# Kernel optimization log

Measured on AMD Instinct MI355X. Metric: run time of the kernel, lower is better.

Reference implementation:

```python
import jax, jax.numpy as jnp
import numpy as np

NUM_PTM_TYPES = 26
NUM_PER_TYPE = 128
TEMPERATURE = 0.07


def setup_inputs() -> dict:
    key = jax.random.key(0)
    k1, k2, k3 = jax.random.split(key, 3)
    N, D = 8192, 256
    x = jax.random.normal(k1, (N, D), dtype=jnp.float32)
    Q = jax.random.randint(k2, (N,), 0, NUM_PTM_TYPES)
    E = jax.random.normal(k3, (NUM_PTM_TYPES * NUM_PER_TYPE, D), dtype=jnp.float32)
    E = E / jnp.linalg.norm(E, axis=1, keepdims=True)  # matches _initialize_embeddings
    return {"x": x, "Q": Q, "E": E, "tau": 1}


def _quantize_grouped(x, Q, E, tau):
    # Vectorized form of the per-PTM-type loop: every type owns an equal-size
    # sub-codebook of NUM_PER_TYPE rows, so gather each token's sub-codebook.
    D = x.shape[-1]
    cb = E.reshape(NUM_PTM_TYPES, NUM_PER_TYPE, D)[Q]          # [N, K, D]
    dot = jnp.einsum('nd,nkd->nk', x, cb) / tau                # [N, K]
    sim = jax.nn.softmax(dot, axis=-1)
    z_q = jnp.einsum('nk,nkd->nd', sim, cb)                    # [N, D]
    idx = jnp.argmax(sim, axis=-1) + Q * NUM_PER_TYPE          # global code index
    return z_q, idx


def _uniform_loss(E):
    K = E.shape[0]
    En = E / jnp.linalg.norm(E, axis=1, keepdims=True)
    sim = En @ En.T                                            # [K, K]
    labels = jnp.arange(K) // NUM_PER_TYPE
    labels_eq = labels[None, :] == labels[:, None]
    eye = jnp.eye(K, dtype=bool)
    sim = jnp.where(eye, -jnp.inf, sim)
    sim_exp = jnp.exp(sim / TEMPERATURE)                       # diagonal -> 0
    sum_exp = jnp.sum(sim_exp, axis=1)
    pos_sum_exp = jnp.sum(sim_exp * labels_eq.astype(sim_exp.dtype), axis=1)
    return -jnp.mean(jnp.log(pos_sum_exp / sum_exp))


def reference(x, Q, E, tau):
    tau = jnp.float32(tau)
    quantized, encoding_indices = _quantize_grouped(x, Q, E, tau)
    loss = jnp.float32(0.0)
    uniform_loss = _uniform_loss(E)
    return quantized, loss, uniform_loss, encoding_indices
```

## Files before the change

### kernel.cpp

```cpp
#include <hip/hip_runtime.h>
#include <hip/hip_bf16.h>

#define NUM_TYPES 26
#define NPT 128
#define DIMS 256
#define K_TOTAL 3328
#define N_TOK 8192
#define INV_TEMP (1.0f/0.07f)
#define TM 16
#define MAX_TILES 32
#define NHIST 32

typedef unsigned short ushort_t;
typedef short bf16x8 __attribute__((ext_vector_type(8)));
typedef float f32x4 __attribute__((ext_vector_type(4)));

__device__ __forceinline__ float wave_reduce_sum(float v){
#pragma unroll
  for (int off = 32; off; off >>= 1) v += __shfl_xor(v, off);
  return v;
}

__device__ __forceinline__ unsigned short f2bf(float f){
  __hip_bfloat16 h = __float2bfloat16(f);
  return __builtin_bit_cast(unsigned short, h);
}

#define GLOAD_LDS16(g, s) \
  __builtin_amdgcn_global_load_lds((__attribute__((address_space(1))) void*)(g), \
                                   (__attribute__((address_space(3))) void*)(s), 16, 0, 0)

#define VMWAIT(N) do{ asm volatile("s_waitcnt vmcnt(" #N ")" ::: "memory"); \
                      __builtin_amdgcn_sched_barrier(0); }while(0)

__global__ __launch_bounds__(256) void prepk(const float* __restrict__ E,
                                             const int* __restrict__ Q,
                                             ushort_t* __restrict__ Enb,
                                             float* __restrict__ EA2,
                                             ushort_t* __restrict__ EC,
                                             int* __restrict__ bh){
  const int t = threadIdx.x;
  const int b = blockIdx.x;
  if (b < 832){
    const int w = t >> 6, l = t & 63;
    const int row = b * 4 + w;
    float4 v = reinterpret_cast<const float4*>(E + (size_t)row * DIMS)[l];
    float ss = v.x*v.x + v.y*v.y + v.z*v.z + v.w*v.w;
    ss = wave_reduce_sum(ss);
    const float inv = 1.0f / sqrtf(ss);
    ushort4 o;
    o.x = f2bf(v.x * inv); o.y = f2bf(v.y * inv);
    o.z = f2bf(v.z * inv); o.w = f2bf(v.w * inv);
    reinterpret_cast<ushort4*>(Enb + (size_t)row * DIMS)[l] = o;
    return;
  }
  if (b < 936){
    const int id = b - 832;
    const int tp = id >> 2, ck = id & 3;
    __shared__ float T[32][260];
    const int row = t >> 3, sub = t & 7;
    const float* src = E + (size_t)(tp*NPT + ck*32 + row) * DIMS;
#pragma unroll
    for (int i = 0; i < 8; ++i){
      const int c4 = sub + 8*i;
      *(f32x4*)(&T[row][c4*4]) = *(const f32x4*)(src + c4*4);
    }
    __syncthreads();
    ushort_t* dst = EC + (size_t)(tp*4 + ck) * 8192;
#pragma unroll
    for (int i = 0; i < 4; ++i){
      const int si = t + i*256;
      const int sec = si >> 8, d = (si >> 2) & 63, s = si & 3;
      const int cb8 = (s ^ ((d >> 1) & 3)) * 8;
      union { bf16x8 v8; ushort_t u[8]; } pk;
#pragma unroll
      for (int j = 0; j < 8; ++j)
        pk.u[j] = f2bf(T[cb8 + j][sec*64 + d]);
      *(bf16x8*)(dst + (size_t)si*8) = pk.v8;
    }
    return;
  }
  if (b < 1144){
    const int id = b - 936;
    const int tp = id >> 3, kt = id & 7;
    float* dst = EA2 + (size_t)tp*32768 + kt*1024;
    const float* src = E + (size_t)tp * NPT * DIMS;
#pragma unroll
    for (int i = 0; i < 16; ++i){
      const int e = i*256 + t;
      const int sec = e >> 10, code = (e >> 3) & 127, j = e & 7;
      dst[sec*8192 + code*8 + j] = src[(size_t)code*DIMS + sec*64 + kt*8 + j];
    }
    return;
  }
  {
    __shared__ int h[NUM_TYPES];
    if (t < NUM_TYPES) h[t] = 0;
    __syncthreads();
    const int c = b - 1144;
    atomicAdd(&h[Q[c*256 + t]], 1);
    __syncthreads();
    if (t < NUM_TYPES) bh[c*NUM_TYPES + t] = h[t];
  }
}

__global__ __launch_bounds__(256) void gramk(const ushort_t* __restrict__ Enb,
                                             const int* __restrict__ Q,
                                             const int* __restrict__ bh,
                                             int* __restrict__ counts,
                                             int* __restrict__ offsets,
                                             int* __restrict__ perm,
                                             float* __restrict__ part){
  const int bi = blockIdx.y, bj = blockIdx.x;
  const int t = threadIdx.x;
  if (bi > bj){
    const int lid = bi*(bi-1)/2 + bj;
    if (lid >= NHIST) return;
    __shared__ int sh_tot[NUM_TYPES], sh_off[NUM_TYPES], sh_cur[NUM_TYPES];
    if (t < NUM_TYPES){
      int s = 0;
      for (int h = 0; h < NHIST; ++h) s += bh[h*NUM_TYPES + t];
      sh_tot[t] = s;
    }
    __syncthreads();
    if (t == 0){
      int s = 0;
      for (int g = 0; g < NUM_TYPES; ++g){ sh_off[g] = s; s += sh_tot[g]; }
    }
    __syncthreads();
    if (t < NUM_TYPES){
      int run = sh_off[t];
      for (int h = 0; h < lid; ++h) run += bh[h*NUM_TYPES + t];
      sh_cur[t] = run;
      if (lid == 0){ counts[t] = sh_tot[t]; offsets[t] = sh_off[t]; }
    }
    __syncthreads();
    const int i = lid*256 + t;
    const int q = Q[i];
    const int pos = atomicAdd(&sh_cur[q], 1);
    perm[pos] = i;
    return;
  }
  __shared__ ushort_t As[128*64];
  __shared__ ushort_t Bs[128*64];
  __shared__ float rs[128][2];
  __shared__ float cs[128][2];
  const int w = t >> 6, l = t & 63;
  const int wr = w >> 1, wc = w & 1;
  const int lrow = l & 15;
  const int lk = (l >> 4) * 8;
  const int hi = l >> 4;

  f32x4 acc[4][4];
#pragma unroll
  for (int m = 0; m < 4; ++m)
#pragma unroll
    for (int n = 0; n < 4; ++n) acc[m][n] = (f32x4){0.f, 0.f, 0.f, 0.f};

  for (int kt = 0; kt < 4; ++kt){
    if (kt) __syncthreads();
#pragma unroll
    for (int p = 0; p < 4; ++p){
      const int cbase = p*256 + w*64;
      const int c = cbase + l;
      const int row = c >> 3;
      const int kcol = (c & 7) * 8;
      const ushort_t* gA = Enb + (size_t)(bi*128 + row) * DIMS + kt*64 + kcol;
      const ushort_t* gB = Enb + (size_t)(bj*128 + row) * DIMS + kt*64 + kcol;
      GLOAD_LDS16(gA, As + (size_t)cbase*8);
      GLOAD_LDS16(gB, Bs + (size_t)cbase*8);
    }
    __syncthreads();
#pragma unroll
    for (int kk = 0; kk < 2; ++kk){
      bf16x8 a[4], b[4];
#pragma unroll
      for (int m = 0; m < 4; ++m)
        a[m] = *reinterpret_cast<const bf16x8*>(&As[(wr*64 + m*16 + lrow)*64 + kk*32 + lk]);
#pragma unroll
      for (int n = 0; n < 4; ++n)
        b[n] = *reinterpret_cast<const bf16x8*>(&Bs[(wc*64 + n*16 + lrow)*64 + kk*32 + lk]);
#pragma unroll
      for (int m = 0; m < 4; ++m)
#pragma unroll
        for (int n = 0; n < 4; ++n)
          acc[m][n] = __builtin_amdgcn_mfma_f32_16x16x32_bf16(a[m], b[n], acc[m][n], 0, 0, 0);
    }
  }

#pragma unroll
  for (int m = 0; m < 4; ++m)
#pragma unroll
    for (int n = 0; n < 4; ++n)
#pragma unroll
      for (int j = 0; j < 4; ++j){
        const int grow = bi*128 + wr*64 + m*16 + hi*4 + j;
        const int gcol = bj*128 + wc*64 + n*16 + lrow;
        const float g = acc[m][n][j];
        acc[m][n][j] = (grow == gcol) ? 0.f : __expf(g * INV_TEMP);
      }

#pragma unroll
  for (int m = 0; m < 4; ++m)
#pragma unroll
    for (int j = 0; j < 4; ++j){
      float s = 0.f;
#pragma unroll
      for (int n = 0; n < 4; ++n) s += acc[m][n][j];
#pragma unroll
      for (int off = 1; off < 16; off <<= 1) s += __shfl_xor(s, off);
      if (lrow == 0) rs[wr*64 + m*16 + hi*4 + j][wc] = s;
    }
  if (bi != bj){
#pragma unroll
    for (int n = 0; n < 4; ++n){
      float c = 0.f;
#pragma unroll
      for (int m = 0; m < 4; ++m)
#pragma unroll
        for (int j = 0; j < 4; ++j) c += acc[m][n][j];
      c += __shfl_xor(c, 16); c += __shfl_xor(c, 32);
      if (hi == 0) cs[wc*64 + n*16 + lrow][wr] = c;
    }
  }
  __syncthreads();
  if (t < 128){
    part[(size_t)bj*K_TOTAL + bi*128 + t] = rs[t][0] + rs[t][1];
    if (bi != bj)
      part[(size_t)bi*K_TOTAL + bj*128 + t] = cs[t][0] + cs[t][1];
  }
}

__device__ __forceinline__ void stageC3(const ushort_t* EC, char* dst, int tp, int ck,
                                        int w, int l){
  const char* src = (const char*)(EC + (size_t)(tp*4 + ck) * 8192) + w*4096;
  char* d = dst + w*4096;
#pragma unroll
  for (int i = 0; i < 4; ++i)
    GLOAD_LDS16(src + i*1024 + l*16, d + i*1024);
}

__global__ __launch_bounds__(256, 4) void quantg(const float* __restrict__ x,
                                                 const float* __restrict__ EA2,
                                                 const ushort_t* __restrict__ EC,
                                                 const float* __restrict__ part,
                                                 const int* __restrict__ counts,
                                                 const int* __restrict__ offsets,
                                                 const int* __restrict__ perm,
                                                 const int* __restrict__ taup,
                                                 float* __restrict__ outZ,
                                                 float* __restrict__ outMisc,
                                                 float* __restrict__ outIdx){
  const int t = threadIdx.x;
  const int tp = blockIdx.x, rb = blockIdx.y;
  __shared__ __align__(16) char arena[37120];

  if (tp == NUM_TYPES){
    if (rb) return;
    float acc = 0.f;
    for (int i = t; i < K_TOTAL; i += 256){
      float s = 0.f;
#pragma unroll
      for (int bb = 0; bb < NUM_TYPES; ++bb) s += part[(size_t)bb*K_TOTAL + i];
      acc += logf(s) - logf(part[(size_t)(i >> 7)*K_TOTAL + i]);
    }
    acc = wave_reduce_sum(acc);
    float* red = (float*)arena;
    if ((t & 63) == 0) red[t >> 6] = acc;
    __syncthreads();
    if (t == 0){ outMisc[0] = 0.f; outMisc[1] = (red[0]+red[1]+red[2]+red[3]) / (float)K_TOTAL; }
    return;
  }

  const int cnt = counts[tp];
  if (rb * TM >= cnt) return;
  const int nt = min(TM, cnt - rb * TM);
  const int off = offsets[tp] + rb * TM;

  char* XA = arena;
  char* PB = arena;
  char* BC = arena;
  char* SB = arena + 32768;

  const int w = t >> 6, l = t & 63;
  const int h  = w >> 1;
  const int cg = w & 1;
  const int tx = l & 15, ty = l >> 4;

  const int ti = *taup;
  const float tau = (ti > 0 && ti < (1 << 23)) ? (float)ti : __int_as_float(ti);
  const float inv_tau = 1.0f / tau;

#pragma unroll
  for (int i = 0; i < 4; ++i){
    const int row = w*4 + i;
    const int tid = (row < nt) ? perm[off + row] : perm[off];
    const int sc = (l & 56) | ((l & 7) ^ (row & 7));
    GLOAD_LDS16(x + (size_t)tid*DIMS + sc*4, XA + row*1024);
  }
  __syncthreads();

  float acc[4][4];
#pragma unroll
  for (int rr = 0; rr < 4; ++rr)
#pragma unroll
    for (int cc = 0; cc < 4; ++cc) acc[rr][cc] = 0.f;

  const float* ea = EA2 + (size_t)tp*32768 + h*16384;
#pragma unroll
  for (int kk = 0; kk < 16; ++kk){
    f32x4 b0[4], b1[4];
#pragma unroll
    for (int cc = 0; cc < 4; ++cc){
      const float* p = ea + (kk >> 3)*8192 + (kk & 7)*1024 + (size_t)(cg*64 + tx + 16*cc)*8;
      b0[cc] = *(const f32x4*)(p);
      b1[cc] = *(const f32x4*)(p + 4);
    }
#pragma unroll
    for (int q = 0; q < 2; ++q){
      f32x4 a[4];
#pragma unroll
      for (int rr = 0; rr < 4; ++rr){
        const int row = rr*4 + ty;
        const int c = (h*32 + kk*2 + q) ^ (row & 7);
        a[rr] = *(const f32x4*)(XA + row*1024 + c*16);
      }
#pragma unroll
      for (int rr = 0; rr < 4; ++rr)
#pragma unroll
        for (int cc = 0; cc < 4; ++cc)
#pragma unroll
          for (int e = 0; e < 4; ++e)
            acc[rr][cc] = fmaf(a[rr][e], (q ? b1 : b0)[cc][e], acc[rr][cc]);
    }
  }
  __syncthreads();

#pragma unroll
  for (int rr = 0; rr < 4; ++rr){
    const int row = rr*4 + ty;
#pragma unroll
    for (int cc = 0; cc < 4; ++cc)
      *(float*)(PB + h*8448 + row*528 + (cg*64 + tx + 16*cc)*4) = acc[rr][cc];
  }
  __syncthreads();

  {
    const int r = t >> 4, s = t & 15;
    f32x4 v0 = (f32x4){0,0,0,0}, v1 = (f32x4){0,0,0,0};
#pragma unroll
    for (int ww = 0; ww < 2; ++ww){
      v0 += *(const f32x4*)(PB + ww*8448 + r*528 + s*32);
      v1 += *(const f32x4*)(PB + ww*8448 + r*528 + s*32 + 16);
    }
    float v[8];
#pragma unroll
    for (int e = 0; e < 4; ++e){ v[e] = v0[e]*inv_tau; v[4+e] = v1[e]*inv_tau; }
    float m = v[0]; int mi = s*8;
#pragma unroll
    for (int j = 1; j < 8; ++j) if (v[j] > m){ m = v[j]; mi = s*8 + j; }
#pragma unroll
    for (int o = 1; o < 16; o <<= 1){
      const float om = __shfl_xor(m, o);
      const int   oi = __shfl_xor(mi, o);
      if (om > m || (om == m && oi < mi)){ m = om; mi = oi; }
    }
    float e8[8]; float sum = 0.f;
#pragma unroll
    for (int j = 0; j < 8; ++j){ e8[j] = __expf(v[j] - m); sum += e8[j]; }
#pragma unroll
    for (int o = 1; o < 16; o <<= 1) sum += __shfl_xor(sum, o);
    const float inv = 1.0f / sum;
    union { bf16x8 v8; ushort_t u[8]; } pk;
#pragma unroll
    for (int j = 0; j < 8; ++j) pk.u[j] = f2bf(e8[j] * inv);
    *(bf16x8*)(SB + r*272 + s*16) = pk.v8;
    if (s == 0 && r < nt)
      outIdx[perm[off + r]] = (float)(mi + tp * NPT);
  }
  __syncthreads();

  stageC3(EC, BC, tp, 0, w, l);
  f32x4 zacc[4];
#pragma unroll
  for (int n = 0; n < 4; ++n) zacc[n] = (f32x4){0,0,0,0};
#pragma unroll
  for (int ck = 0; ck < 4; ++ck){
    if (ck < 3) stageC3(EC, BC + ((ck+1)&1)*16384, tp, ck+1, w, l);
    if (ck < 3)      { VMWAIT(4); }
    else             { VMWAIT(0); }
    const bf16x8 af = *(const bf16x8*)(SB + tx*272 + ck*64 + ty*16);
    const char* bbuf = BC + (ck&1)*16384 + w*4096;
#pragma unroll
    for (int n = 0; n < 4; ++n){
      const int d = n*16 + tx;
      const int slot = ty ^ ((d >> 1) & 3);
      const bf16x8 bf = *(const bf16x8*)(bbuf + d*64 + slot*16);
      zacc[n] = __builtin_amdgcn_mfma_f32_16x16x32_bf16(af, bf, zacc[n], 0, 0, 0);
    }
  }
#pragma unroll
  for (int n = 0; n < 4; ++n)
#pragma unroll
    for (int j = 0; j < 4; ++j){
      const int row = ty*4 + j;
      if (row < nt)
        outZ[(size_t)perm[off + row]*DIMS + w*64 + n*16 + tx] = zacc[n][j];
    }
}

extern "C" void kernel_launch(void* const* d_in, const int* in_sizes, int n_in,
                              void* d_out, int out_size, void* d_ws, size_t ws_size,
                              hipStream_t stream){
  const float* x  = (const float*)d_in[0];
  const int*   Q  = (const int*)d_in[1];
  const float* E  = (const float*)d_in[2];
  const int* taup = (const int*)d_in[3];

  float* outZ    = (float*)d_out;
  float* outMisc = outZ + (size_t)N_TOK * DIMS;
  float* outIdx  = outMisc + 2;

  char* wsp = (char*)d_ws;
  ushort_t* Enb = (ushort_t*)wsp;
  float* part   = (float*)(wsp + 1703936);
  float* EA2    = (float*)(wsp + 2050048);
  ushort_t* EC  = (ushort_t*)(wsp + 5457920);
  int* bh       = (int*)(wsp + 7161856);
  int* counts   = (int*)(wsp + 7165184);
  int* offsets  = (int*)(wsp + 7165312);
  int* perm     = (int*)(wsp + 7165440);

  prepk<<<1176, 256, 0, stream>>>(E, Q, Enb, EA2, EC, bh);
  gramk<<<dim3(26, 26), 256, 0, stream>>>(Enb, Q, bh, counts, offsets, perm, part);
  quantg<<<dim3(NUM_TYPES + 1, MAX_TILES), 256, 0, stream>>>(x, EA2, EC, part,
                                                             counts, offsets, perm,
                                                             taup, outZ, outMisc, outIdx);
}
```

Measured before the change: 45.87 us.

## Move codebook layout prep into gram kernel idle blocks and parallelize loss reduction

The EC and EA2 codebook re-layout blocks move out of the first kernel and into otherwise idle lower-triangle blocks of the gram kernel, with the grid grown by one row so there are enough spare blocks. This shortens the critical first kernel and overlaps the layout work with the gram matmul. The final uniform-loss reduction is split across 26 blocks, and a threadfence plus atomic counter picks a last block to combine the partial sums, replacing a single serial block. The exchange is an extra memset launch and atomics, and gram tiles now use a shared arena sized for the largest use.

```diff
diff --git a/kernel.cpp b/kernel.cpp
--- a/kernel.cpp
+++ b/kernel.cpp
@@ -36,8 +36,6 @@
 __global__ __launch_bounds__(256) void prepk(const float* __restrict__ E,
                                              const int* __restrict__ Q,
                                              ushort_t* __restrict__ Enb,
-                                             float* __restrict__ EA2,
-                                             ushort_t* __restrict__ EC,
                                              int* __restrict__ bh){
   const int t = threadIdx.x;
   const int b = blockIdx.x;
@@ -54,97 +52,105 @@
     reinterpret_cast<ushort4*>(Enb + (size_t)row * DIMS)[l] = o;
     return;
   }
-  if (b < 936){
-    const int id = b - 832;
-    const int tp = id >> 2, ck = id & 3;
-    __shared__ float T[32][260];
-    const int row = t >> 3, sub = t & 7;
-    const float* src = E + (size_t)(tp*NPT + ck*32 + row) * DIMS;
-#pragma unroll
-    for (int i = 0; i < 8; ++i){
-      const int c4 = sub + 8*i;
-      *(f32x4*)(&T[row][c4*4]) = *(const f32x4*)(src + c4*4);
-    }
-    __syncthreads();
-    ushort_t* dst = EC + (size_t)(tp*4 + ck) * 8192;
-#pragma unroll
-    for (int i = 0; i < 4; ++i){
-      const int si = t + i*256;
-      const int sec = si >> 8, d = (si >> 2) & 63, s = si & 3;
-      const int cb8 = (s ^ ((d >> 1) & 3)) * 8;
-      union { bf16x8 v8; ushort_t u[8]; } pk;
-#pragma unroll
-      for (int j = 0; j < 8; ++j)
-        pk.u[j] = f2bf(T[cb8 + j][sec*64 + d]);
-      *(bf16x8*)(dst + (size_t)si*8) = pk.v8;
-    }
-    return;
-  }
-  if (b < 1144){
-    const int id = b - 936;
-    const int tp = id >> 3, kt = id & 7;
-    float* dst = EA2 + (size_t)tp*32768 + kt*1024;
-    const float* src = E + (size_t)tp * NPT * DIMS;
-#pragma unroll
-    for (int i = 0; i < 16; ++i){
-      const int e = i*256 + t;
-      const int sec = e >> 10, code = (e >> 3) & 127, j = e & 7;
-      dst[sec*8192 + code*8 + j] = src[(size_t)code*DIMS + sec*64 + kt*8 + j];
-    }
-    return;
-  }
   {
     __shared__ int h[NUM_TYPES];
     if (t < NUM_TYPES) h[t] = 0;
     __syncthreads();
-    const int c = b - 1144;
+    const int c = b - 832;
     atomicAdd(&h[Q[c*256 + t]], 1);
     __syncthreads();
     if (t < NUM_TYPES) bh[c*NUM_TYPES + t] = h[t];
   }
 }
 
-__global__ __launch_bounds__(256) void gramk(const ushort_t* __restrict__ Enb,
+__global__ __launch_bounds__(256) void gramk(const float* __restrict__ E,
+                                             const ushort_t* __restrict__ Enb,
                                              const int* __restrict__ Q,
                                              const int* __restrict__ bh,
+                                             float* __restrict__ EA2,
+                                             ushort_t* __restrict__ EC,
                                              int* __restrict__ counts,
                                              int* __restrict__ offsets,
                                              int* __restrict__ perm,
                                              float* __restrict__ part){
   const int bi = blockIdx.y, bj = blockIdx.x;
   const int t = threadIdx.x;
+  __shared__ __align__(16) char sharena[34816];
+
   if (bi > bj){
     const int lid = bi*(bi-1)/2 + bj;
-    if (lid >= NHIST) return;
-    __shared__ int sh_tot[NUM_TYPES], sh_off[NUM_TYPES], sh_cur[NUM_TYPES];
-    if (t < NUM_TYPES){
-      int s = 0;
-      for (int h = 0; h < NHIST; ++h) s += bh[h*NUM_TYPES + t];
-      sh_tot[t] = s;
-    }
-    __syncthreads();
-    if (t == 0){
-      int s = 0;
-      for (int g = 0; g < NUM_TYPES; ++g){ sh_off[g] = s; s += sh_tot[g]; }
-    }
-    __syncthreads();
-    if (t < NUM_TYPES){
-      int run = sh_off[t];
-      for (int h = 0; h < lid; ++h) run += bh[h*NUM_TYPES + t];
-      sh_cur[t] = run;
-      if (lid == 0){ counts[t] = sh_tot[t]; offsets[t] = sh_off[t]; }
-    }
-    __syncthreads();
-    const int i = lid*256 + t;
-    const int q = Q[i];
-    const int pos = atomicAdd(&sh_cur[q], 1);
-    perm[pos] = i;
+    if (lid < NHIST){
+      __shared__ int sh_tot[NUM_TYPES], sh_off[NUM_TYPES], sh_cur[NUM_TYPES];
+      if (t < NUM_TYPES){
+        int s = 0;
+        for (int h = 0; h < NHIST; ++h) s += bh[h*NUM_TYPES + t];
+        sh_tot[t] = s;
+      }
+      __syncthreads();
+      if (t == 0){
+        int s = 0;
+        for (int g = 0; g < NUM_TYPES; ++g){ sh_off[g] = s; s += sh_tot[g]; }
+      }
+      __syncthreads();
+      if (t < NUM_TYPES){
+        int run = sh_off[t];
+        for (int h = 0; h < lid; ++h) run += bh[h*NUM_TYPES + t];
+        sh_cur[t] = run;
+        if (lid == 0){ counts[t] = sh_tot[t]; offsets[t] = sh_off[t]; }
+      }
+      __syncthreads();
+      const int i = lid*256 + t;
+      const int q = Q[i];
+      const int pos = atomicAdd(&sh_cur[q], 1);
+      perm[pos] = i;
+      return;
+    }
+    if (lid < 136){
+      const int id = lid - 32;
+      const int tp = id >> 2, ck = id & 3;
+      float (*T)[260] = (float(*)[260])sharena;
+      const int row = t >> 3, sub = t & 7;
+      const float* src = E + (size_t)(tp*NPT + ck*32 + row) * DIMS;
+#pragma unroll
+      for (int i = 0; i < 8; ++i){
+        const int c4 = sub + 8*i;
+        *(f32x4*)(&T[row][c4*4]) = *(const f32x4*)(src + c4*4);
+      }
+      __syncthreads();
+      ushort_t* dst = EC + (size_t)(tp*4 + ck) * 8192;
+#pragma unroll
+      for (int i = 0; i < 4; ++i){
+        const int si = t + i*256;
+        const int sec = si >> 8, d = (si >> 2) & 63, s = si & 3;
+        const int cb8 = (s ^ ((d >> 1) & 3)) * 8;
+        union { bf16x8 v8; ushort_t u[8]; } pk;
+#pragma unroll
+        for (int j = 0; j < 8; ++j)
+          pk.u[j] = f2bf(T[cb8 + j][sec*64 + d]);
+        *(bf16x8*)(dst + (size_t)si*8) = pk.v8;
+      }
+      return;
+    }
+    if (lid < 344){
+      const int id = lid - 136;
+      const int tp = id >> 3, kt = id & 7;
+      float* dst = EA2 + (size_t)tp*32768 + kt*1024;
+      const float* src = E + (size_t)tp * NPT * DIMS;
+#pragma unroll
+      for (int i = 0; i < 16; ++i){
+        const int e = i*256 + t;
+        const int sec = e >> 10, code = (e >> 3) & 127, j = e & 7;
+        dst[sec*8192 + code*8 + j] = src[(size_t)code*DIMS + sec*64 + kt*8 + j];
+      }
+      return;
+    }
     return;
   }
-  __shared__ ushort_t As[128*64];
-  __shared__ ushort_t Bs[128*64];
-  __shared__ float rs[128][2];
-  __shared__ float cs[128][2];
+
+  ushort_t* As = (ushort_t*)sharena;
+  ushort_t* Bs = (ushort_t*)(sharena + 16384);
+  float (*rs)[2] = (float(*)[2])(sharena + 32768);
+  float (*cs)[2] = (float(*)[2])(sharena + 33792);
   const int w = t >> 6, l = t & 63;
   const int wr = w >> 1, wc = w & 1;
   const int lrow = l & 15;
@@ -248,6 +254,8 @@
                                                  const int* __restrict__ offsets,
                                                  const int* __restrict__ perm,
                                                  const int* __restrict__ taup,
+                                                 float* __restrict__ ppart,
+                                                 int* __restrict__ lossCnt,
                                                  float* __restrict__ outZ,
                                                  float* __restrict__ outMisc,
                                                  float* __restrict__ outIdx){
@@ -256,19 +264,32 @@
   __shared__ __align__(16) char arena[37120];
 
   if (tp == NUM_TYPES){
-    if (rb) return;
-    float acc = 0.f;
-    for (int i = t; i < K_TOTAL; i += 256){
+    if (rb >= NUM_TYPES) return;
+    float a = 0.f;
+    if (t < 128){
+      const int i = rb*128 + t;
       float s = 0.f;
 #pragma unroll
       for (int bb = 0; bb < NUM_TYPES; ++bb) s += part[(size_t)bb*K_TOTAL + i];
-      acc += logf(s) - logf(part[(size_t)(i >> 7)*K_TOTAL + i]);
-    }
-    acc = wave_reduce_sum(acc);
+      a = logf(s) - logf(part[(size_t)rb*K_TOTAL + i]);
+    }
+    a = wave_reduce_sum(a);
     float* red = (float*)arena;
-    if ((t & 63) == 0) red[t >> 6] = acc;
+    if ((t & 63) == 0 && t < 128) red[t >> 6] = a;
     __syncthreads();
-    if (t == 0){ outMisc[0] = 0.f; outMisc[1] = (red[0]+red[1]+red[2]+red[3]) / (float)K_TOTAL; }
+    if (t == 0){
+      atomicExch(&ppart[rb], red[0] + red[1]);
+      __threadfence();
+      const int n = atomicAdd(lossCnt, 1);
+      if (n == NUM_TYPES - 1){
+        float s = 0.f;
+#pragma unroll
+        for (int bb = 0; bb < NUM_TYPES; ++bb)
+          s += atomicAdd(&ppart[bb], 0.0f);
+        outMisc[0] = 0.f;
+        outMisc[1] = s / (float)K_TOTAL;
+      }
+    }
     return;
   }
 
@@ -429,11 +450,16 @@
   int* bh       = (int*)(wsp + 7161856);
   int* counts   = (int*)(wsp + 7165184);
   int* offsets  = (int*)(wsp + 7165312);
-  int* perm     = (int*)(wsp + 7165440);
-
-  prepk<<<1176, 256, 0, stream>>>(E, Q, Enb, EA2, EC, bh);
-  gramk<<<dim3(26, 26), 256, 0, stream>>>(Enb, Q, bh, counts, offsets, perm, part);
+  float* ppart  = (float*)(wsp + 7165440);
+  int* lossCnt  = (int*)(wsp + 7165568);
+  int* perm     = (int*)(wsp + 7165696);
+
+  hipMemsetAsync(lossCnt, 0, sizeof(int), stream);
+  prepk<<<864, 256, 0, stream>>>(E, Q, Enb, bh);
+  gramk<<<dim3(26, 27), 256, 0, stream>>>(E, Enb, Q, bh, EA2, EC,
+                                          counts, offsets, perm, part);
   quantg<<<dim3(NUM_TYPES + 1, MAX_TILES), 256, 0, stream>>>(x, EA2, EC, part,
                                                              counts, offsets, perm,
-                                                             taup, outZ, outMisc, outIdx);
-}
+                                                             taup, ppart, lossCnt,
+                                                             outZ, outMisc, outIdx);
+}
```

Result: slower. 48.21 us (+5.1%).
